# Kernel tuning notes

Hardware: AMD Instinct MI355X
Metric: run time of the kernel (lower is better)

The kernel has to match this reference:

```python
import jax, jax.numpy as jnp
import numpy as np

PATCH = 16
H_RES, W_RES = 512, 512
PREFIX = 8
NUM_HEADS = 12
DIM = 768
GAUSS_STD = 5.0


def gauss_addition():
    # n_patches = (w//16, h//16); addition[(i,j),(k,l)] = exp(-((i-k)^2+(j-l)^2)/(2*std^2))
    d1, d2 = W_RES // PATCH, H_RES // PATCH  # (32, 32)
    inv2s2 = 1.0 / (2.0 * GAUSS_STD * GAUSS_STD)
    i = jnp.arange(d1, dtype=jnp.float32)
    j = jnp.arange(d2, dtype=jnp.float32)
    Ai = jnp.exp(-((i[:, None] - i[None, :]) ** 2) * inv2s2)  # [d1,d1]
    Aj = jnp.exp(-((j[:, None] - j[None, :]) ** 2) * inv2s2)  # [d2,d2]
    add = jnp.einsum('ik,jl->ijkl', Ai, Aj).reshape(d1 * d2, d1 * d2)
    # zero rows/cols for the prefix tokens (prepended)
    return jnp.pad(add, ((PREFIX, 0), (PREFIX, 0)))  # [N,N]


def setup_inputs() -> dict:
    key = jax.random.key(0)
    ks = jax.random.split(key, 5)
    N = (W_RES // PATCH) * (H_RES // PATCH) + PREFIX  # 1032
    B, C = 8, DIM
    x = jax.random.normal(ks[0], (B, N, C), dtype=jnp.float32)
    w_qkv = jax.random.normal(ks[1], (3 * C, C), dtype=jnp.float32) * 0.02
    b_qkv = jax.random.normal(ks[2], (3 * C,), dtype=jnp.float32) * 0.02
    w_proj = jax.random.normal(ks[3], (C, C), dtype=jnp.float32) * 0.02
    b_proj = jax.random.normal(ks[4], (C,), dtype=jnp.float32) * 0.02
    return {'x': x, 'w_qkv': w_qkv, 'b_qkv': b_qkv, 'w_proj': w_proj, 'b_proj': b_proj}


def reference(x, w_qkv, b_qkv, w_proj, b_proj):
    B, N, C = x.shape
    H = NUM_HEADS
    hd = C // H
    scale = hd ** -0.5
    qkv = x @ w_qkv.T + b_qkv              # [B,N,3C]
    k = qkv[..., C:2 * C].reshape(B, N, H, hd)
    v = qkv[..., 2 * C:].reshape(B, N, H, hd)
    add = gauss_addition().astype(x.dtype)  # [N,N], broadcast over B,H
    scores = jnp.einsum('bnhd,bmhd->bhnm', k, k) * scale + add
    attn = jax.nn.softmax(scores, axis=-1)
    out = jnp.einsum('bhnm,bmhd->bnhd', attn, v).reshape(B, N, C)
    return out @ w_proj.T + b_proj
```

## Files before the change

kernel.cpp:

```cpp
#include <hip/hip_runtime.h>
#include <hip/hip_bf16.h>

typedef unsigned short u16;
typedef __bf16 bf16x8 __attribute__((ext_vector_type(8)));
typedef __bf16 bf16x4 __attribute__((ext_vector_type(4)));
typedef float f32x4 __attribute__((ext_vector_type(4)));

#define DEVI __device__ __forceinline__

#if __has_builtin(__builtin_amdgcn_exp2f)
#define EXP2 __builtin_amdgcn_exp2f
#else
#define EXP2 exp2f
#endif

constexpr int Bn = 8, Nn = 1032, Cn = 768, Hn = 12, HDn = 64;
constexpr int NQPc = 1088;
constexpr int NVM = 1088;
constexpr int MTOT = Bn * Nn;
constexpr int MPAD = 8320;
constexpr int KVN = 1536;
constexpr int PFXc = 8;
constexpr int NPADQ = NVM - Nn;
constexpr float SCALEc = 0.125f;
constexpr float LOG2Ec = 1.4426950408889634f;
constexpr float C1c = SCALEc * LOG2Ec;
constexpr float INV2S2c = 0.02f;
constexpr float K2c = INV2S2c * LOG2Ec;

constexpr size_t OFF_XB  = 0;
constexpr size_t SZ_XB   = (size_t)MPAD * Cn * 2;
constexpr size_t OFF_AT  = OFF_XB;
constexpr size_t OFF_WKV = OFF_XB + SZ_XB;
constexpr size_t SZ_WKV  = (size_t)KVN * Cn * 2;
constexpr size_t OFF_WP  = OFF_WKV + SZ_WKV;
constexpr size_t SZ_WP   = (size_t)Cn * Cn * 2;
constexpr size_t OFF_K   = OFF_WP + SZ_WP;
constexpr size_t SZ_K    = (size_t)Bn * Hn * NQPc * HDn * 2;
constexpr size_t OFF_V   = OFF_K + SZ_K;
constexpr size_t SZ_V    = (size_t)Bn * Hn * HDn * NVM * 2;

DEVI u16 f2bf(float f) {
  __bf16 h = (__bf16)f;
  return *reinterpret_cast<u16*>(&h);
}

DEVI void glds16(const void* g, void* l) {
  __builtin_amdgcn_global_load_lds((const __attribute__((address_space(1))) void*)g,
                                   (__attribute__((address_space(3))) void*)l, 16, 0, 0);
}

__global__ __launch_bounds__(256) void prep_kernel(
    const float* __restrict__ x, const float* __restrict__ wqkv,
    const float* __restrict__ wproj, u16* __restrict__ xb,
    u16* __restrict__ wkvb, u16* __restrict__ wpb,
    u16* __restrict__ khead, u16* __restrict__ vT) {
  const int n1 = MPAD * Cn / 4, n2 = KVN * Cn / 4, n3 = Cn * Cn / 4;
  const int z1 = 96 * 448;
  const int z2 = 6144 * 7;
  const int nc = n1 + n2 + n3;
  const int tot = nc + z1 + z2;
  for (int i = blockIdx.x * blockDim.x + threadIdx.x; i < tot; i += gridDim.x * blockDim.x) {
    if (i < nc) {
      const float* src; u16* dst;
      if (i < n1) {
        int e = i * 4;
        src = (e < MTOT * Cn) ? (x + e) : nullptr;
        dst = xb + e;
      } else if (i < n1 + n2) {
        int e = (i - n1) * 4;
        src = wqkv + Cn * Cn + e;
        dst = wkvb + e;
      } else {
        int e = (i - n1 - n2) * 4;
        src = wproj + e;
        dst = wpb + e;
      }
      float4 f = src ? *(const float4*)src : make_float4(0.f, 0.f, 0.f, 0.f);
      *(ushort4*)dst = make_ushort4(f2bf(f.x), f2bf(f.y), f2bf(f.z), f2bf(f.w));
    } else if (i < nc + z1) {
      int j = i - nc, bh = j / 448, c = j - bh * 448;
      char* dst = (char*)khead + ((size_t)bh * NQPc + Nn) * HDn * 2 + c * 16;
      *(ushort4*)dst = make_ushort4(0, 0, 0, 0);
      *(ushort4*)(dst + 8) = make_ushort4(0, 0, 0, 0);
    } else {
      int j = i - nc - z1, st = j / 7, c = j - st * 7;
      char* dst = (char*)vT + ((size_t)st * NVM + Nn) * 2 + c * 16;
      *(ushort4*)dst = make_ushort4(0, 0, 0, 0);
      *(ushort4*)(dst + 8) = make_ushort4(0, 0, 0, 0);
    }
  }
}

DEVI void gemm_mainloop(const u16* __restrict__ A, const u16* __restrict__ Bm,
                        int m0, int n0, char* sA, char* sB, f32x4 (&acc)[4][4]) {
  const int tid = threadIdx.x, lane = tid & 63, w = tid >> 6;
  const int ln = lane & 15, lg = lane >> 4;
  const int wm = (w >> 1) * 64, wn = (w & 1) * 64;
  for (int kt = 0; kt < 12; ++kt) {
#pragma unroll
    for (int i = 0; i < 4; ++i) {
      const int c = i * 256 + tid, r = c >> 3, cb = c & 7, gcb = cb ^ (r & 7);
      const char* ga = (const char*)(A + (size_t)(m0 + r) * Cn + kt * 64) + gcb * 16;
      glds16(ga, sA + i * 4096 + w * 1024);
      const char* gb = (const char*)(Bm + (size_t)(n0 + r) * Cn + kt * 64) + gcb * 16;
      glds16(gb, sB + i * 4096 + w * 1024);
    }
    __syncthreads();
#pragma unroll
    for (int ks = 0; ks < 2; ++ks) {
      bf16x8 af[4], bfr[4];
#pragma unroll
      for (int s = 0; s < 4; ++s) {
        const int ra = wm + s * 16 + ln;
        af[s] = *(const bf16x8*)(sA + ra * 128 + (((ks * 4 + lg) ^ (ra & 7)) << 4));
        const int rb = wn + s * 16 + ln;
        bfr[s] = *(const bf16x8*)(sB + rb * 128 + (((ks * 4 + lg) ^ (rb & 7)) << 4));
      }
#pragma unroll
      for (int s = 0; s < 4; ++s)
#pragma unroll
        for (int t = 0; t < 4; ++t)
          acc[s][t] = __builtin_amdgcn_mfma_f32_16x16x32_bf16(af[s], bfr[t], acc[s][t], 0, 0, 0);
    }
    __syncthreads();
  }
}

__global__ __launch_bounds__(256) void kv_gemm(
    const u16* __restrict__ xb, const u16* __restrict__ wkvb,
    const float* __restrict__ bqkv, u16* __restrict__ khead, u16* __restrict__ vT) {
  __shared__ __align__(16) char smem[34816];
  char* sA = smem;
  char* sB = smem + 16384;
  const int bid = blockIdx.x;
  const int xcd = bid & 7, loc = bid >> 3;
  const int wgid = (xcd < 4) ? xcd * 98 + loc : 392 + (xcd - 4) * 97 + loc;
  const int m0 = (wgid / 12) * 128, n0 = (wgid % 12) * 128;
  f32x4 acc[4][4] = {};
  gemm_mainloop(xb, wkvb, m0, n0, sA, sB, acc);
  const int tid = threadIdx.x, lane = tid & 63, w = tid >> 6;
  const int ln = lane & 15, lg = lane >> 4;
  const int wm = (w >> 1) * 64, wn = (w & 1) * 64;
  const bool isV = (n0 >= Cn);
  u16* T = (u16*)smem;
  __syncthreads();
  if (!isV) {
#pragma unroll
    for (int t = 0; t < 4; ++t) {
      const int c = wn + t * 16 + ln;
      const float bias = bqkv[Cn + n0 + c];
#pragma unroll
      for (int s = 0; s < 4; ++s)
#pragma unroll
        for (int r = 0; r < 4; ++r)
          T[(wm + s * 16 + lg * 4 + r) * 136 + c] = f2bf(acc[s][t][r] + bias);
    }
    __syncthreads();
    const int h0 = n0 >> 6;
#pragma unroll
    for (int i = 0; i < 8; ++i) {
      const int runid = w * 64 + i * 8 + (lane >> 3);
      const int mloc = runid >> 1, hh = runid & 1;
      const int m = m0 + mloc;
      if (m < MTOT) {
        const int b = m / Nn, nr = m - b * Nn;
        const int d0 = (lane & 7) * 8;
        *(uint4*)&khead[((size_t)(b * Hn + h0 + hh) * NQPc + nr) * HDn + d0] =
            *(const uint4*)&T[mloc * 136 + hh * 64 + d0];
      }
    }
  } else {
#pragma unroll
    for (int t = 0; t < 4; ++t) {
      const int c = wn + t * 16 + ln;
      const float bias = bqkv[Cn + n0 + c];
#pragma unroll
      for (int s = 0; s < 4; ++s)
#pragma unroll
        for (int r = 0; r < 4; ++r)
          T[c * 136 + wm + s * 16 + lg * 4 + r] = f2bf(acc[s][t][r] + bias);
    }
    __syncthreads();
    const int vch0 = n0 - Cn;
#pragma unroll
    for (int i = 0; i < 8; ++i) {
      const int c = w * 32 + i * 4 + lg;
      const int vch = vch0 + c, h = vch >> 6, d = vch & 63;
      const int m = m0 + ln * 8;
      if (m < MTOT) {
        const int b = m / Nn, nr = m - b * Nn;
        *(uint4*)&vT[((size_t)(b * Hn + h) * HDn + d) * NVM + nr] =
            *(const uint4*)&T[c * 136 + ln * 8];
      }
    }
  }
}

__global__ __launch_bounds__(256, 4) void attn_kernel(
    const u16* __restrict__ khead, const u16* __restrict__ vT, u16* __restrict__ attn) {
  __shared__ __align__(16) char sK[2][8192];
  __shared__ __align__(16) char sV[2][8192];
  __shared__ __align__(16) char sP[4][2048];
  const int tid = threadIdx.x, lane = tid & 63, w = tid >> 6;
  const int ln = lane & 15, lg = lane >> 4;
  const int bid = blockIdx.x;

  bf16x8 ones8;
#pragma unroll
  for (int i = 0; i < 8; ++i) ones8[i] = (__bf16)1.0f;

  if (bid < 768) {
    const int xcd = bid & 7, loc = bid >> 3;
    const int lid = xcd * 96 + loc;
    const int qt = lid & 7, bh = lid >> 3;
    const int qb = PFXc + qt * 128 + w * 32;

    bf16x8 qf[2][2];
#pragma unroll
    for (int qg = 0; qg < 2; ++qg) {
      const char* qp = (const char*)(khead + ((size_t)bh * NQPc + qb + qg * 16 + ln) * HDn);
#pragma unroll
      for (int kc = 0; kc < 2; ++kc)
        qf[qg][kc] = *(const bf16x8*)(qp + kc * 64 + lg * 16);
    }

    const float c2 = EXP2(-2.0f * K2c);
    float ajr[2][8];
    float a0[2], a1[2], a2[2], fr[2];
#pragma unroll
    for (int qg = 0; qg < 2; ++qg) {
      const int pq = qt * 128 + w * 32 + qg * 16 + ln;
      const int iq = pq >> 5, jq = pq & 31;
#pragma unroll
      for (int t = 0; t < 8; ++t) {
        const int jm = (lg * 4 - 8 + (t >> 2) * 16 + (t & 3)) & 31;
        const float d = (float)(jq - jm);
        ajr[qg][t] = EXP2(-d * d * K2c);
      }
      const float d1 = (float)(iq + 1), d0 = (float)iq, dm = (float)(iq - 1);
      a0[qg] = EXP2(-d1 * d1 * K2c) * LOG2Ec;
      a1[qg] = EXP2(-d0 * d0 * K2c) * LOG2Ec;
      a2[qg] = EXP2(-dm * dm * K2c) * LOG2Ec;
      fr[qg] = EXP2((2.0f * (float)iq - 3.0f) * K2c);
    }

    const char* ksrc = (const char*)(khead + (size_t)bh * NQPc * HDn);
    const char* vsrc = (const char*)(vT + (size_t)bh * HDn * NVM);

#define STAGE(buf, mb) do { \
  _Pragma("unroll") for (int i_ = 0; i_ < 2; ++i_) { \
    const int c_ = i_ * 256 + tid, r_ = c_ >> 3, gcb_ = (c_ & 7) ^ (r_ & 7); \
    glds16(ksrc + (size_t)((mb) + r_) * 128 + gcb_ * 16, sK[buf] + i_ * 4096 + w * 1024); \
    glds16(vsrc + (size_t)r_ * (NVM * 2) + (mb) * 2 + gcb_ * 16, sV[buf] + i_ * 4096 + w * 1024); \
  } } while (0)

    f32x4 oacc[4][2] = {};
    f32x4 dacc[2] = {};
    STAGE(0, 0);

    for (int mc = 0; mc < 17; ++mc) {
      const int cur = mc & 1;
      const int mb = mc * 64;
      if (mc < 16) {
        STAGE(cur ^ 1, mb + 64);
        asm volatile("s_waitcnt vmcnt(4)" ::: "memory");
      } else {
        asm volatile("s_waitcnt vmcnt(0)" ::: "memory");
      }
      __builtin_amdgcn_sched_barrier(0);
      __builtin_amdgcn_s_barrier();
      __builtin_amdgcn_sched_barrier(0);

      f32x4 sacc[4][2] = {};
      __builtin_amdgcn_s_setprio(1);
#pragma unroll
      for (int ms = 0; ms < 4; ++ms) {
        const int r = ms * 16 + ln;
#pragma unroll
        for (int kc = 0; kc < 2; ++kc) {
          bf16x8 kf = *(const bf16x8*)(sK[cur] + r * 128 + (((kc * 4 + lg) ^ (r & 7)) << 4));
          sacc[ms][0] = __builtin_amdgcn_mfma_f32_16x16x32_bf16(kf, qf[0][kc], sacc[ms][0], 0, 0, 0);
          sacc[ms][1] = __builtin_amdgcn_mfma_f32_16x16x32_bf16(kf, qf[1][kc], sacc[ms][1], 0, 0, 0);
        }
      }
      __builtin_amdgcn_s_setprio(0);

      bf16x8 pf[2][2];
#pragma unroll
      for (int qg = 0; qg < 2; ++qg) {
        const float b0 = (mc == 0) ? 0.f : a0[qg];
        const float b1 = (mc == 16) ? 0.f : a1[qg];
        const float b2 = (mc == 16) ? 0.f : a2[qg];
#pragma unroll
        for (int ms = 0; ms < 4; ++ms) {
          float al;
          if (ms == 0)      al = (lg < 2) ? b0 : b1;
          else if (ms == 1) al = b1;
          else if (ms == 2) al = (lg < 2) ? b1 : b2;
          else              al = b2;
          const int t0 = (ms & 1) * 4;
          const float p0 = EXP2(fmaf(sacc[ms][qg][0], C1c, al * ajr[qg][t0 + 0]));
          const float p1 = EXP2(fmaf(sacc[ms][qg][1], C1c, al * ajr[qg][t0 + 1]));
          const float p2 = EXP2(fmaf(sacc[ms][qg][2], C1c, al * ajr[qg][t0 + 2]));
          const float p3 = EXP2(fmaf(sacc[ms][qg][3], C1c, al * ajr[qg][t0 + 3]));
          bf16x4 pk;
          pk[0] = (__bf16)p0; pk[1] = (__bf16)p1; pk[2] = (__bf16)p2; pk[3] = (__bf16)p3;
          *(bf16x4*)(sP[w] + ln * 128 + ((ms * 32 + lg * 8) ^ ((ln & 7) << 4))) = pk;
        }
#pragma unroll
        for (int km = 0; km < 2; ++km)
          pf[qg][km] = *(const bf16x8*)(sP[w] + ln * 128 +
                                        ((km * 64 + lg * 16) ^ ((ln & 7) << 4)));
        a0[qg] = a2[qg];
        a1[qg] = a2[qg] * fr[qg]; fr[qg] *= c2;
        a2[qg] = a1[qg] * fr[qg]; fr[qg] *= c2;
      }

      __builtin_amdgcn_s_setprio(1);
      dacc[0] = __builtin_amdgcn_mfma_f32_16x16x32_bf16(pf[0][0], ones8, dacc[0], 0, 0, 0);
      dacc[0] = __builtin_amdgcn_mfma_f32_16x16x32_bf16(pf[0][1], ones8, dacc[0], 0, 0, 0);
      dacc[1] = __builtin_amdgcn_mfma_f32_16x16x32_bf16(pf[1][0], ones8, dacc[1], 0, 0, 0);
      dacc[1] = __builtin_amdgcn_mfma_f32_16x16x32_bf16(pf[1][1], ones8, dacc[1], 0, 0, 0);
#pragma unroll
      for (int ds = 0; ds < 4; ++ds) {
        const int r = ds * 16 + ln;
#pragma unroll
        for (int km = 0; km < 2; ++km) {
          bf16x8 vf = *(const bf16x8*)(sV[cur] + r * 128 + (((km * 4 + lg) ^ (r & 7)) << 4));
          oacc[ds][0] = __builtin_amdgcn_mfma_f32_16x16x32_bf16(pf[0][km], vf, oacc[ds][0], 0, 0, 0);
          oacc[ds][1] = __builtin_amdgcn_mfma_f32_16x16x32_bf16(pf[1][km], vf, oacc[ds][1], 0, 0, 0);
        }
      }
      __builtin_amdgcn_s_setprio(0);
      __builtin_amdgcn_sched_barrier(0);
      __builtin_amdgcn_s_barrier();
      __builtin_amdgcn_sched_barrier(0);
    }
#undef STAGE

    const int b = bh / Hn, h = bh - b * Hn;
#pragma unroll
    for (int qg = 0; qg < 2; ++qg) {
#pragma unroll
      for (int r = 0; r < 4; ++r) {
        const int qo = qb + qg * 16 + lg * 4 + r;
        const float dinv = 1.0f / (dacc[qg][r] - (float)NPADQ);
#pragma unroll
        for (int ds = 0; ds < 4; ++ds)
          attn[((size_t)(b * Nn + qo)) * Cn + h * HDn + ds * 16 + ln] =
              f2bf(oacc[ds][qg][r] * dinv);
      }
    }
  } else {
    const int i = bid - 768;
    const int bh = (i & 7) * 12 + (i >> 3);
    const char* ksrc = (const char*)(khead + (size_t)bh * NQPc * HDn);
    const char* vsrc = (const char*)(vT + (size_t)bh * HDn * NVM);
    const char* qp = (const char*)(khead + ((size_t)bh * NQPc + ln) * HDn);
    bf16x8 qf[2];
    qf[0] = *(const bf16x8*)(qp + lg * 16);
    qf[1] = *(const bf16x8*)(qp + 64 + lg * 16);

    f32x4 oacc[4] = {};
    f32x4 dacc = {};
    for (int mc = w; mc < 17; mc += 4) {
      const int mb = mc * 64;
      f32x4 sacc[4] = {};
#pragma unroll
      for (int ms = 0; ms < 4; ++ms) {
        const char* kp = ksrc + (size_t)(mb + ms * 16 + ln) * 128 + lg * 16;
        bf16x8 kf0 = *(const bf16x8*)(kp);
        bf16x8 kf1 = *(const bf16x8*)(kp + 64);
        sacc[ms] = __builtin_amdgcn_mfma_f32_16x16x32_bf16(kf0, qf[0], sacc[ms], 0, 0, 0);
        sacc[ms] = __builtin_amdgcn_mfma_f32_16x16x32_bf16(kf1, qf[1], sacc[ms], 0, 0, 0);
      }
#pragma unroll
      for (int ms = 0; ms < 4; ++ms) {
        bf16x4 pk;
        pk[0] = (__bf16)EXP2(sacc[ms][0] * C1c);
        pk[1] = (__bf16)EXP2(sacc[ms][1] * C1c);
        pk[2] = (__bf16)EXP2(sacc[ms][2] * C1c);
        pk[3] = (__bf16)EXP2(sacc[ms][3] * C1c);
        *(bf16x4*)(sP[w] + ln * 128 + ((ms * 32 + lg * 8) ^ ((ln & 7) << 4))) = pk;
      }
      bf16x8 pf[2];
#pragma unroll
      for (int km = 0; km < 2; ++km)
        pf[km] = *(const bf16x8*)(sP[w] + ln * 128 + ((km * 64 + lg * 16) ^ ((ln & 7) << 4)));
      dacc = __builtin_amdgcn_mfma_f32_16x16x32_bf16(pf[0], ones8, dacc, 0, 0, 0);
      dacc = __builtin_amdgcn_mfma_f32_16x16x32_bf16(pf[1], ones8, dacc, 0, 0, 0);
#pragma unroll
      for (int ds = 0; ds < 4; ++ds) {
        const char* vp = vsrc + (size_t)(ds * 16 + ln) * (NVM * 2) + mb * 2 + lg * 16;
#pragma unroll
        for (int km = 0; km < 2; ++km) {
          bf16x8 vf = *(const bf16x8*)(vp + km * 64);
          oacc[ds] = __builtin_amdgcn_mfma_f32_16x16x32_bf16(pf[km], vf, oacc[ds], 0, 0, 0);
        }
      }
    }
    char* sKf = (char*)sK;
    char* sVf = (char*)sV;
    __syncthreads();
#pragma unroll
    for (int ds = 0; ds < 4; ++ds)
      *(f32x4*)(sKf + (((w * 4 + ds) * 64 + lane) << 4)) = oacc[ds];
    *(f32x4*)(sVf + ((w * 64 + lane) << 4)) = dacc;
    __syncthreads();
    f32x4 osum = {}, dsum = {};
#pragma unroll
    for (int wp = 0; wp < 4; ++wp) {
      osum += *(const f32x4*)(sKf + (((wp * 4 + w) * 64 + lane) << 4));
      dsum += *(const f32x4*)(sVf + ((wp * 64 + lane) << 4));
    }
    const int b = bh / Hn, h = bh - b * Hn;
#pragma unroll
    for (int r = 0; r < 4; ++r) {
      const int q = lg * 4 + r;
      if (q < PFXc)
        attn[((size_t)(b * Nn + q)) * Cn + h * HDn + w * 16 + ln] =
            f2bf(osum[r] / (dsum[r] - (float)NPADQ));
    }
  }
}

__global__ __launch_bounds__(256) void proj_gemm(
    const u16* __restrict__ at, const u16* __restrict__ wpb,
    const float* __restrict__ bproj, float* __restrict__ out) {
  __shared__ __align__(16) char sA[16384];
  __shared__ __align__(16) char sB[16384];
  const int bid = blockIdx.x;
  const int xcd = bid & 7, loc = bid >> 3;
  const int wgid = (xcd < 6) ? xcd * 49 + loc : 294 + (xcd - 6) * 48 + loc;
  const int m0 = (wgid / 6) * 128, n0 = (wgid % 6) * 128;
  f32x4 acc[4][4] = {};
  gemm_mainloop(at, wpb, m0, n0, sA, sB, acc);
  const int tid = threadIdx.x, lane = tid & 63, w = tid >> 6;
  const int ln = lane & 15, lg = lane >> 4;
  const int wm = (w >> 1) * 64, wn = (w & 1) * 64;
#pragma unroll
  for (int t = 0; t < 4; ++t) {
    const int n = n0 + wn + t * 16 + ln;
    const float bias = bproj[n];
#pragma unroll
    for (int s = 0; s < 4; ++s) {
#pragma unroll
      for (int r = 0; r < 4; ++r) {
        const int m = m0 + wm + s * 16 + lg * 4 + r;
        if (m < MTOT) out[(size_t)m * Cn + n] = acc[s][t][r] + bias;
      }
    }
  }
}

extern "C" void kernel_launch(void* const* d_in, const int* in_sizes, int n_in,
                              void* d_out, int out_size, void* d_ws, size_t ws_size,
                              hipStream_t stream) {
  const float* x     = (const float*)d_in[0];
  const float* wqkv  = (const float*)d_in[1];
  const float* bqkv  = (const float*)d_in[2];
  const float* wproj = (const float*)d_in[3];
  const float* bproj = (const float*)d_in[4];
  char* ws = (char*)d_ws;
  u16* xb    = (u16*)(ws + OFF_XB);
  u16* wkvb  = (u16*)(ws + OFF_WKV);
  u16* wpb   = (u16*)(ws + OFF_WP);
  u16* khead = (u16*)(ws + OFF_K);
  u16* vT    = (u16*)(ws + OFF_V);
  u16* attn  = (u16*)(ws + OFF_AT);

  prep_kernel<<<2048, 256, 0, stream>>>(x, wqkv, wproj, xb, wkvb, wpb, khead, vT);
  kv_gemm<<<780, 256, 0, stream>>>(xb, wkvb, bqkv, khead, vT);
  attn_kernel<<<864, 256, 0, stream>>>(khead, vT, attn);
  proj_gemm<<<390, 256, 0, stream>>>(attn, wpb, bproj, (float*)d_out);
}
```

Measured before the change: 123.6 us.

## Software-pipeline QK^T one tile ahead of softmax and PV in attention loop

Restructures the attention main loop so the QK^T MFMAs for the next key tile run before the exp/softmax and PV work of the current tile. K and V loads are staged separately so each is fetched only when needed, and the loop is unrolled by two with ping-pong score accumulators. The aim is to hide the exp/VALU latency behind MFMA work. The change also drops the min-blocks-per-CU hint in launch_bounds, which frees registers for the extra accumulators but may lower occupancy.

Result: faster. 119.6 us, median of 2 (-3.2%).

```diff
diff --git a/kernel.cpp b/kernel.cpp
--- a/kernel.cpp
+++ b/kernel.cpp
@@ -197,7 +197,7 @@
   }
 }
 
-__global__ __launch_bounds__(256, 4) void attn_kernel(
+__global__ __launch_bounds__(256) void attn_kernel(
     const u16* __restrict__ khead, const u16* __restrict__ vT, u16* __restrict__ attn) {
   __shared__ __align__(16) char sK[2][8192];
   __shared__ __align__(16) char sV[2][8192];
@@ -209,6 +209,7 @@
   bf16x8 ones8;
 #pragma unroll
   for (int i = 0; i < 8; ++i) ones8[i] = (__bf16)1.0f;
+  const f32x4 fzero = {0.f, 0.f, 0.f, 0.f};
 
   if (bid < 768) {
     const int xcd = bid & 7, loc = bid >> 3;
@@ -248,96 +249,122 @@
     const char* ksrc = (const char*)(khead + (size_t)bh * NQPc * HDn);
     const char* vsrc = (const char*)(vT + (size_t)bh * HDn * NVM);
 
-#define STAGE(buf, mb) do { \
+#define STAGE_K(buf, mb) do { \
   _Pragma("unroll") for (int i_ = 0; i_ < 2; ++i_) { \
     const int c_ = i_ * 256 + tid, r_ = c_ >> 3, gcb_ = (c_ & 7) ^ (r_ & 7); \
     glds16(ksrc + (size_t)((mb) + r_) * 128 + gcb_ * 16, sK[buf] + i_ * 4096 + w * 1024); \
+  } } while (0)
+#define STAGE_V(buf, mb) do { \
+  _Pragma("unroll") for (int i_ = 0; i_ < 2; ++i_) { \
+    const int c_ = i_ * 256 + tid, r_ = c_ >> 3, gcb_ = (c_ & 7) ^ (r_ & 7); \
     glds16(vsrc + (size_t)r_ * (NVM * 2) + (mb) * 2 + gcb_ * 16, sV[buf] + i_ * 4096 + w * 1024); \
   } } while (0)
-
+#define QK_STEP(kb, SACC) do { \
+  _Pragma("unroll") \
+  for (int z_ = 0; z_ < 4; ++z_) { SACC[z_][0] = fzero; SACC[z_][1] = fzero; } \
+  __builtin_amdgcn_s_setprio(1); \
+  _Pragma("unroll") \
+  for (int ms_ = 0; ms_ < 4; ++ms_) { \
+    const int r_ = ms_ * 16 + ln; \
+    _Pragma("unroll") \
+    for (int kc_ = 0; kc_ < 2; ++kc_) { \
+      bf16x8 kf_ = *(const bf16x8*)(sK[kb] + r_ * 128 + (((kc_ * 4 + lg) ^ (r_ & 7)) << 4)); \
+      SACC[ms_][0] = __builtin_amdgcn_mfma_f32_16x16x32_bf16(kf_, qf[0][kc_], SACC[ms_][0], 0, 0, 0); \
+      SACC[ms_][1] = __builtin_amdgcn_mfma_f32_16x16x32_bf16(kf_, qf[1][kc_], SACC[ms_][1], 0, 0, 0); \
+    } } \
+  __builtin_amdgcn_s_setprio(0); } while (0)
+#define P_PHASE(SACC, is0v, is16v) do { \
+  _Pragma("unroll") \
+  for (int qg_ = 0; qg_ < 2; ++qg_) { \
+    const float b0_ = (is0v) ? 0.f : a0[qg_]; \
+    const float b1_ = (is16v) ? 0.f : a1[qg_]; \
+    const float b2_ = (is16v) ? 0.f : a2[qg_]; \
+    _Pragma("unroll") \
+    for (int ms_ = 0; ms_ < 4; ++ms_) { \
+      float al_; \
+      if (ms_ == 0)      al_ = (lg < 2) ? b0_ : b1_; \
+      else if (ms_ == 1) al_ = b1_; \
+      else if (ms_ == 2) al_ = (lg < 2) ? b1_ : b2_; \
+      else               al_ = b2_; \
+      const int t0_ = (ms_ & 1) * 4; \
+      const float p0_ = EXP2(fmaf(SACC[ms_][qg_][0], C1c, al_ * ajr[qg_][t0_ + 0])); \
+      const float p1_ = EXP2(fmaf(SACC[ms_][qg_][1], C1c, al_ * ajr[qg_][t0_ + 1])); \
+      const float p2_ = EXP2(fmaf(SACC[ms_][qg_][2], C1c, al_ * ajr[qg_][t0_ + 2])); \
+      const float p3_ = EXP2(fmaf(SACC[ms_][qg_][3], C1c, al_ * ajr[qg_][t0_ + 3])); \
+      bf16x4 pk_; \
+      pk_[0] = (__bf16)p0_; pk_[1] = (__bf16)p1_; pk_[2] = (__bf16)p2_; pk_[3] = (__bf16)p3_; \
+      *(bf16x4*)(sP[w] + ln * 128 + ((ms_ * 32 + lg * 8) ^ ((ln & 7) << 4))) = pk_; \
+    } \
+    _Pragma("unroll") \
+    for (int km_ = 0; km_ < 2; ++km_) \
+      pf[qg_][km_] = *(const bf16x8*)(sP[w] + ln * 128 + ((km_ * 64 + lg * 16) ^ ((ln & 7) << 4))); \
+    a0[qg_] = a2[qg_]; \
+    a1[qg_] = a2[qg_] * fr[qg_]; fr[qg_] *= c2; \
+    a2[qg_] = a1[qg_] * fr[qg_]; fr[qg_] *= c2; \
+  } } while (0)
+#define PV_STEP(vb) do { \
+  __builtin_amdgcn_s_setprio(1); \
+  dacc[0] = __builtin_amdgcn_mfma_f32_16x16x32_bf16(pf[0][0], ones8, dacc[0], 0, 0, 0); \
+  dacc[0] = __builtin_amdgcn_mfma_f32_16x16x32_bf16(pf[0][1], ones8, dacc[0], 0, 0, 0); \
+  dacc[1] = __builtin_amdgcn_mfma_f32_16x16x32_bf16(pf[1][0], ones8, dacc[1], 0, 0, 0); \
+  dacc[1] = __builtin_amdgcn_mfma_f32_16x16x32_bf16(pf[1][1], ones8, dacc[1], 0, 0, 0); \
+  _Pragma("unroll") \
+  for (int ds_ = 0; ds_ < 4; ++ds_) { \
+    const int r_ = ds_ * 16 + ln; \
+    _Pragma("unroll") \
+    for (int km_ = 0; km_ < 2; ++km_) { \
+      bf16x8 vf_ = *(const bf16x8*)(sV[vb] + r_ * 128 + (((km_ * 4 + lg) ^ (r_ & 7)) << 4)); \
+      oacc[ds_][0] = __builtin_amdgcn_mfma_f32_16x16x32_bf16(pf[0][km_], vf_, oacc[ds_][0], 0, 0, 0); \
+      oacc[ds_][1] = __builtin_amdgcn_mfma_f32_16x16x32_bf16(pf[1][km_], vf_, oacc[ds_][1], 0, 0, 0); \
+    } } \
+  __builtin_amdgcn_s_setprio(0); } while (0)
+#define BARRIER() do { __builtin_amdgcn_sched_barrier(0); \
+  __builtin_amdgcn_s_barrier(); __builtin_amdgcn_sched_barrier(0); } while (0)
+
+    f32x4 saccA[4][2], saccB[4][2];
     f32x4 oacc[4][2] = {};
     f32x4 dacc[2] = {};
-    STAGE(0, 0);
-
-    for (int mc = 0; mc < 17; ++mc) {
-      const int cur = mc & 1;
-      const int mb = mc * 64;
-      if (mc < 16) {
-        STAGE(cur ^ 1, mb + 64);
+    bf16x8 pf[2][2];
+
+    STAGE_K(0, 0); STAGE_V(0, 0); STAGE_K(1, 64);
+    asm volatile("s_waitcnt vmcnt(4)" ::: "memory");
+    BARRIER();
+    QK_STEP(0, saccA);
+
+    for (int d = 0; d < 8; ++d) {
+      BARRIER();
+      STAGE_K(0, (2 * d + 2) * 64);
+      STAGE_V(1, (2 * d + 1) * 64);
+      asm volatile("s_waitcnt vmcnt(4)" ::: "memory");
+      BARRIER();
+      QK_STEP(1, saccB);
+      P_PHASE(saccA, (d == 0), false);
+      PV_STEP(0);
+      BARRIER();
+      if (d < 7) {
+        STAGE_K(1, (2 * d + 3) * 64);
+        STAGE_V(0, (2 * d + 2) * 64);
         asm volatile("s_waitcnt vmcnt(4)" ::: "memory");
       } else {
-        asm volatile("s_waitcnt vmcnt(0)" ::: "memory");
-      }
-      __builtin_amdgcn_sched_barrier(0);
-      __builtin_amdgcn_s_barrier();
-      __builtin_amdgcn_sched_barrier(0);
-
-      f32x4 sacc[4][2] = {};
-      __builtin_amdgcn_s_setprio(1);
-#pragma unroll
-      for (int ms = 0; ms < 4; ++ms) {
-        const int r = ms * 16 + ln;
-#pragma unroll
-        for (int kc = 0; kc < 2; ++kc) {
-          bf16x8 kf = *(const bf16x8*)(sK[cur] + r * 128 + (((kc * 4 + lg) ^ (r & 7)) << 4));
-          sacc[ms][0] = __builtin_amdgcn_mfma_f32_16x16x32_bf16(kf, qf[0][kc], sacc[ms][0], 0, 0, 0);
-          sacc[ms][1] = __builtin_amdgcn_mfma_f32_16x16x32_bf16(kf, qf[1][kc], sacc[ms][1], 0, 0, 0);
-        }
-      }
-      __builtin_amdgcn_s_setprio(0);
-
-      bf16x8 pf[2][2];
-#pragma unroll
-      for (int qg = 0; qg < 2; ++qg) {
-        const float b0 = (mc == 0) ? 0.f : a0[qg];
-        const float b1 = (mc == 16) ? 0.f : a1[qg];
-        const float b2 = (mc == 16) ? 0.f : a2[qg];
-#pragma unroll
-        for (int ms = 0; ms < 4; ++ms) {
-          float al;
-          if (ms == 0)      al = (lg < 2) ? b0 : b1;
-          else if (ms == 1) al = b1;
-          else if (ms == 2) al = (lg < 2) ? b1 : b2;
-          else              al = b2;
-          const int t0 = (ms & 1) * 4;
-          const float p0 = EXP2(fmaf(sacc[ms][qg][0], C1c, al * ajr[qg][t0 + 0]));
-          const float p1 = EXP2(fmaf(sacc[ms][qg][1], C1c, al * ajr[qg][t0 + 1]));
-          const float p2 = EXP2(fmaf(sacc[ms][qg][2], C1c, al * ajr[qg][t0 + 2]));
-          const float p3 = EXP2(fmaf(sacc[ms][qg][3], C1c, al * ajr[qg][t0 + 3]));
-          bf16x4 pk;
-          pk[0] = (__bf16)p0; pk[1] = (__bf16)p1; pk[2] = (__bf16)p2; pk[3] = (__bf16)p3;
-          *(bf16x4*)(sP[w] + ln * 128 + ((ms * 32 + lg * 8) ^ ((ln & 7) << 4))) = pk;
-        }
-#pragma unroll
-        for (int km = 0; km < 2; ++km)
-          pf[qg][km] = *(const bf16x8*)(sP[w] + ln * 128 +
-                                        ((km * 64 + lg * 16) ^ ((ln & 7) << 4)));
-        a0[qg] = a2[qg];
-        a1[qg] = a2[qg] * fr[qg]; fr[qg] *= c2;
-        a2[qg] = a1[qg] * fr[qg]; fr[qg] *= c2;
-      }
-
-      __builtin_amdgcn_s_setprio(1);
-      dacc[0] = __builtin_amdgcn_mfma_f32_16x16x32_bf16(pf[0][0], ones8, dacc[0], 0, 0, 0);
-      dacc[0] = __builtin_amdgcn_mfma_f32_16x16x32_bf16(pf[0][1], ones8, dacc[0], 0, 0, 0);
-      dacc[1] = __builtin_amdgcn_mfma_f32_16x16x32_bf16(pf[1][0], ones8, dacc[1], 0, 0, 0);
-      dacc[1] = __builtin_amdgcn_mfma_f32_16x16x32_bf16(pf[1][1], ones8, dacc[1], 0, 0, 0);
-#pragma unroll
-      for (int ds = 0; ds < 4; ++ds) {
-        const int r = ds * 16 + ln;
-#pragma unroll
-        for (int km = 0; km < 2; ++km) {
-          bf16x8 vf = *(const bf16x8*)(sV[cur] + r * 128 + (((km * 4 + lg) ^ (r & 7)) << 4));
-          oacc[ds][0] = __builtin_amdgcn_mfma_f32_16x16x32_bf16(pf[0][km], vf, oacc[ds][0], 0, 0, 0);
-          oacc[ds][1] = __builtin_amdgcn_mfma_f32_16x16x32_bf16(pf[1][km], vf, oacc[ds][1], 0, 0, 0);
-        }
-      }
-      __builtin_amdgcn_s_setprio(0);
-      __builtin_amdgcn_sched_barrier(0);
-      __builtin_amdgcn_s_barrier();
-      __builtin_amdgcn_sched_barrier(0);
-    }
-#undef STAGE
+        STAGE_V(0, 16 * 64);
+        asm volatile("s_waitcnt vmcnt(2)" ::: "memory");
+      }
+      BARRIER();
+      QK_STEP(0, saccA);
+      P_PHASE(saccB, false, false);
+      PV_STEP(1);
+    }
+    asm volatile("s_waitcnt vmcnt(0)" ::: "memory");
+    BARRIER();
+    P_PHASE(saccA, false, true);
+    PV_STEP(0);
+
+#undef STAGE_K
+#undef STAGE_V
+#undef QK_STEP
+#undef P_PHASE
+#undef PV_STEP
+#undef BARRIER
 
     const int b = bh / Hn, h = bh - b * Hn;
 #pragma unroll
```
